# Kernel tuning notes

Hardware: AMD Instinct MI355X
Metric: run time of the kernel (lower is better)

Reference implementation:

```python
import jax, jax.numpy as jnp
import numpy as np

B, S, H = 4, 256, 768
NUM_BASIC = 4
NUM_REL = 32            # labels 1..31 are real edges, 0 = no edge
NUM_ALL = 2 * NUM_REL   # bidir: forward slots 0..31, reverse slots 33..63


def setup_inputs() -> dict:
    key = jax.random.key(0)
    k1, k2, k3, k4, k5 = jax.random.split(key, 5)
    hidden_states = jax.random.normal(k1, (B, S, H), dtype=jnp.float32)
    rels = jax.random.randint(k2, (B, S, S), 0, NUM_REL, dtype=jnp.int32)
    # xavier-ish init scale for params
    basic_matrix = jax.random.normal(k3, (NUM_BASIC, H, H), dtype=jnp.float32) * 0.02
    rel_weight = jax.random.normal(k4, (NUM_ALL, NUM_BASIC), dtype=jnp.float32) * 0.1
    self_weight = jax.random.normal(k5, (H, H), dtype=jnp.float32) * 0.02  # Linear weight (out,in)
    return {"hidden_states": hidden_states, "rels": rels,
            "basic_matrix": basic_matrix, "rel_weight": rel_weight,
            "self_weight": self_weight}


def reference(hidden_states, rels, basic_matrix, rel_weight, self_weight):
    dt = hidden_states.dtype
    # forward-direction one-hot relation tensor [B, NUM_ALL, S, S], masked where rels == 0
    fwd_mask = (rels > 0).astype(dt)                                   # [B,S,S]
    fwd_oh = jax.nn.one_hot(rels, NUM_ALL, axis=1, dtype=dt) * fwd_mask[:, None]
    # reverse direction (bidir): labels shifted by NUM_REL, zeroed where no edge
    rev_rels_raw = jnp.transpose(rels, (0, 2, 1))
    rev_rels = jnp.where(rev_rels_raw > 0, rev_rels_raw + NUM_REL, 0)  # {0} U {33..63}
    rev_mask = (rev_rels > 0).astype(dt)
    rev_oh = jax.nn.one_hot(rev_rels, NUM_ALL, axis=1, dtype=dt) * rev_mask[:, None]
    rel_tensor = fwd_oh + rev_oh                                       # [B,R,S,S]

    # basis decomposition: per-relation transform [R, H, H]
    rel_matrix = jnp.einsum('rb,bio->rio', rel_weight, basic_matrix)
    # per-relation transformed hidden states [B,R,S,H]
    r_hidden = jnp.einsum('bsi,rio->brso', hidden_states, rel_matrix)
    # adjacency aggregation [B,R,S,H]
    r_ctx = jnp.einsum('brij,brjo->brio', rel_tensor, r_hidden)
    # mean over neighbors (clamp count at 1)
    num_neighbors = jnp.maximum(rel_tensor.sum(-1), 1.0)               # [B,R,S]
    r_ctx = r_ctx / num_neighbors[..., None]
    context = r_ctx.sum(axis=1)                                        # [B,S,H]
    self_layer = hidden_states @ self_weight.T
    return self_layer + context
```

## Files before the change

kernel.cpp:

```cpp
#include <hip/hip_runtime.h>
#include <stdint.h>

typedef unsigned short u16;
typedef unsigned int u32;
typedef __attribute__((ext_vector_type(8))) short short8;
typedef __attribute__((ext_vector_type(4))) float float4v;

#define Bb 4
#define Ss 256
#define Hh 768
#define NBASIC 4
#define NALL 64

__device__ __forceinline__ float b2f(u16 h) {
    u32 u = ((u32)h) << 16;
    float f;
    __builtin_memcpy(&f, &u, 4);
    return f;
}
__device__ __forceinline__ u16 f2b(float f) {
    u32 u;
    __builtin_memcpy(&u, &f, 4);
    u = (u + 0x7fffu + ((u >> 16) & 1u)) >> 16;
    return (u16)u;
}

__device__ __forceinline__ int detect_bf16(const u32* __restrict__ hw) {
    int cnt = 0;
#pragma unroll
    for (int k = 0; k < 64; ++k) {
        const int e = (int)((hw[k] >> 7) & 0xFFu);
        cnt += (e >= 100 && e <= 140) ? 1 : 0;
    }
    return cnt >= 40;
}

__global__ __launch_bounds__(256) void k_prep(const void* __restrict__ h_raw,
                                              const void* __restrict__ basic_raw,
                                              const void* __restrict__ selfw_raw,
                                              const void* __restrict__ relw_raw,
                                              const int* __restrict__ rels,
                                              u16* __restrict__ hbf,
                                              u16* __restrict__ swbf,
                                              u16* __restrict__ basicT,
                                              u16* __restrict__ hT,
                                              u16* __restrict__ coefC) {
    __shared__ u16 tile[32][33];
    __shared__ float srelw[256];
    __shared__ u32 hist[NALL];

    const int blk = blockIdx.x;
    const int t = threadIdx.x;
    const int bf = detect_bf16((const u32*)h_raw);

    if (blk < 3072) {
        const int i = blk * 256 + t;
        hbf[i] = bf ? ((const u16*)h_raw)[i] : f2b(((const float*)h_raw)[i]);
    } else if (blk < 5376) {
        const int i = (blk - 3072) * 256 + t;
        swbf[i] = bf ? ((const u16*)selfw_raw)[i] : f2b(((const float*)selfw_raw)[i]);
    } else if (blk < 7680) {
        const int r = blk - 5376;
        const int o0 = (r % 24) * 32, i0 = ((r / 24) % 24) * 32, q = r / 576;
        const int tx = t & 31, ty = t >> 5;
        const size_t base = (size_t)q * Hh * Hh;
#pragma unroll
        for (int rr = 0; rr < 4; ++rr) {
            const size_t idx = base + (size_t)(i0 + ty + 8 * rr) * Hh + o0 + tx;
            tile[ty + 8 * rr][tx] = bf ? ((const u16*)basic_raw)[idx]
                                       : f2b(((const float*)basic_raw)[idx]);
        }
        __syncthreads();
#pragma unroll
        for (int rr = 0; rr < 4; ++rr)
            basicT[base + (size_t)(o0 + ty + 8 * rr) * Hh + i0 + tx] = tile[tx][ty + 8 * rr];
    } else if (blk < 8448) {
        const int r = blk - 7680;
        const int o0 = (r % 24) * 32, i0 = ((r / 24) % 8) * 32, b = r / 192;
        const int tx = t & 31, ty = t >> 5;
#pragma unroll
        for (int rr = 0; rr < 4; ++rr) {
            const size_t idx = ((size_t)b * Ss + i0 + ty + 8 * rr) * Hh + o0 + tx;
            tile[ty + 8 * rr][tx] = bf ? ((const u16*)h_raw)[idx]
                                       : f2b(((const float*)h_raw)[idx]);
        }
        __syncthreads();
#pragma unroll
        for (int rr = 0; rr < 4; ++rr)
            hT[((size_t)b * Hh + o0 + ty + 8 * rr) * Ss + i0 + tx] = tile[tx][ty + 8 * rr];
    } else {
        const int r = blk - 8448;
        const int i = r & 255, b = r >> 8;
        srelw[t] = bf ? b2f(((const u16*)relw_raw)[t]) : ((const float*)relw_raw)[t];
        if (t < NALL) hist[t] = 0u;
        __syncthreads();
        const int rf = rels[(b * Ss + i) * Ss + t];
        const int rc = rels[(b * Ss + t) * Ss + i];
        if (rf > 0) atomicAdd(&hist[rf], 1u);
        if (rc > 0) atomicAdd(&hist[rc + 32], 1u);
        __syncthreads();
        float c0 = 0.f, c1 = 0.f, c2 = 0.f, c3 = 0.f;
        if (rf > 0) {
            const float inv = 1.0f / (float)hist[rf];
            c0 += srelw[rf * 4 + 0] * inv; c1 += srelw[rf * 4 + 1] * inv;
            c2 += srelw[rf * 4 + 2] * inv; c3 += srelw[rf * 4 + 3] * inv;
        }
        if (rc > 0) {
            const int rr = rc + 32;
            const float inv = 1.0f / (float)hist[rr];
            c0 += srelw[rr * 4 + 0] * inv; c1 += srelw[rr * 4 + 1] * inv;
            c2 += srelw[rr * 4 + 2] * inv; c3 += srelw[rr * 4 + 3] * inv;
        }
        const size_t base = ((size_t)(b * 4) * Ss + i) * Ss + t;
        coefC[base]                    = f2b(c0);
        coefC[base + (size_t)Ss * Ss]     = f2b(c1);
        coefC[base + (size_t)2 * Ss * Ss] = f2b(c2);
        coefC[base + (size_t)3 * Ss * Ss] = f2b(c3);
    }
}

__global__ __launch_bounds__(256) void k_gemmP(const u16* __restrict__ coefC,
                                               const u16* __restrict__ hT,
                                               u16* __restrict__ pooled) {
    constexpr int LDT = 72;
    __shared__ u16 As[64 * LDT];
    __shared__ u16 Bs[64 * LDT];

    const int bk = blockIdx.z;
    const int b = bk >> 2;
    const int i0 = blockIdx.y * 64;
    const int o0 = blockIdx.x * 64;
    const int t = threadIdx.x;
    const int row = t >> 2, kk = (t & 3) * 16;
    const int w = t >> 6, l = t & 63, quad = l >> 4, l16 = l & 15;

    float4v acc[4];
#pragma unroll
    for (int c = 0; c < 4; ++c) acc[c] = (float4v){0.f, 0.f, 0.f, 0.f};

    const u16* aB = coefC + ((size_t)bk * Ss + i0 + row) * Ss + kk;
    const u16* bB = hT + ((size_t)b * Hh + o0 + row) * Ss + kk;

    uint4 a0 = *(const uint4*)aB;
    uint4 a1 = *(const uint4*)(aB + 8);
    uint4 b0 = *(const uint4*)bB;
    uint4 b1 = *(const uint4*)(bB + 8);

    for (int s = 0; s < 4; ++s) {
        __syncthreads();
        *(uint4*)(&As[row * LDT + kk]) = a0;
        *(uint4*)(&As[row * LDT + kk + 8]) = a1;
        *(uint4*)(&Bs[row * LDT + kk]) = b0;
        *(uint4*)(&Bs[row * LDT + kk + 8]) = b1;
        __syncthreads();
        if (s + 1 < 4) {
            a0 = *(const uint4*)(aB + (s + 1) * 64);
            a1 = *(const uint4*)(aB + (s + 1) * 64 + 8);
            b0 = *(const uint4*)(bB + (s + 1) * 64);
            b1 = *(const uint4*)(bB + (s + 1) * 64 + 8);
        }
#pragma unroll
        for (int k2 = 0; k2 < 64; k2 += 32) {
            const short8 af = *(const short8*)(&As[(16 * w + l16) * LDT + k2 + quad * 8]);
#pragma unroll
            for (int c = 0; c < 4; ++c) {
                const short8 bfr = *(const short8*)(&Bs[(16 * c + l16) * LDT + k2 + quad * 8]);
                acc[c] = __builtin_amdgcn_mfma_f32_16x16x32_bf16(af, bfr, acc[c], 0, 0, 0);
            }
        }
    }

#pragma unroll
    for (int c = 0; c < 4; ++c)
#pragma unroll
        for (int r = 0; r < 4; ++r) {
            const int il = 16 * w + quad * 4 + r;
            const int ol = 16 * c + l16;
            pooled[((size_t)bk * Ss + i0 + il) * Hh + o0 + ol] = f2b(acc[c][r]);
        }
}

__global__ __launch_bounds__(256) void k_gemmO(const u16* __restrict__ hbf,
                                               const u16* __restrict__ pooled,
                                               const u16* __restrict__ basicT,
                                               const u16* __restrict__ swbf,
                                               float* __restrict__ partial) {
    constexpr int LDT = 72;
    __shared__ u16 As[64 * LDT];
    __shared__ u16 Bs[64 * LDT];

    const int z = blockIdx.z;
    const int b = z & 3, q = z >> 2;
    const int i0 = blockIdx.y * 64;
    const int o0 = blockIdx.x * 64;
    const int t = threadIdx.x;
    const int row = t >> 2, kk = (t & 3) * 16;
    const int w = t >> 6, l = t & 63, quad = l >> 4, l16 = l & 15;

    float4v acc[4];
#pragma unroll
    for (int c = 0; c < 4; ++c) acc[c] = (float4v){0.f, 0.f, 0.f, 0.f};

    const u16* aB = (q < 4) ? pooled + (((size_t)(b * 4 + q)) * Ss + i0 + row) * Hh + kk
                            : hbf + ((size_t)b * Ss + i0 + row) * Hh + kk;
    const u16* bB = (q < 4) ? basicT + ((size_t)q * Hh + o0 + row) * Hh + kk
                            : swbf + (size_t)(o0 + row) * Hh + kk;

    uint4 a0 = *(const uint4*)aB;
    uint4 a1 = *(const uint4*)(aB + 8);
    uint4 b0 = *(const uint4*)bB;
    uint4 b1 = *(const uint4*)(bB + 8);

    for (int s = 0; s < 12; ++s) {
        __syncthreads();
        *(uint4*)(&As[row * LDT + kk]) = a0;
        *(uint4*)(&As[row * LDT + kk + 8]) = a1;
        *(uint4*)(&Bs[row * LDT + kk]) = b0;
        *(uint4*)(&Bs[row * LDT + kk + 8]) = b1;
        __syncthreads();
        if (s + 1 < 12) {
            a0 = *(const uint4*)(aB + (s + 1) * 64);
            a1 = *(const uint4*)(aB + (s + 1) * 64 + 8);
            b0 = *(const uint4*)(bB + (s + 1) * 64);
            b1 = *(const uint4*)(bB + (s + 1) * 64 + 8);
        }
#pragma unroll
        for (int k2 = 0; k2 < 64; k2 += 32) {
            const short8 af = *(const short8*)(&As[(16 * w + l16) * LDT + k2 + quad * 8]);
#pragma unroll
            for (int c = 0; c < 4; ++c) {
                const short8 bfr = *(const short8*)(&Bs[(16 * c + l16) * LDT + k2 + quad * 8]);
                acc[c] = __builtin_amdgcn_mfma_f32_16x16x32_bf16(af, bfr, acc[c], 0, 0, 0);
            }
        }
    }

#pragma unroll
    for (int c = 0; c < 4; ++c)
#pragma unroll
        for (int r = 0; r < 4; ++r) {
            const int il = 16 * w + quad * 4 + r;
            const int ol = 16 * c + l16;
            partial[((size_t)z * Ss + i0 + il) * Hh + o0 + ol] = acc[c][r];
        }
}

__global__ __launch_bounds__(256) void k_reduce(const float* __restrict__ partial,
                                                const void* __restrict__ h_raw,
                                                void* __restrict__ outv) {
    const int bf = detect_bf16((const u32*)h_raw);
    const size_t idx = ((size_t)blockIdx.x * 256 + threadIdx.x) * 4;
    const size_t slice = (size_t)Bb * Ss * Hh;
    float4 s = *(const float4*)(partial + idx);
#pragma unroll
    for (int q = 1; q < 5; ++q) {
        const float4 p = *(const float4*)(partial + q * slice + idx);
        s.x += p.x; s.y += p.y; s.z += p.z; s.w += p.w;
    }
    if (bf) {
        const u32 lo = (u32)f2b(s.x) | ((u32)f2b(s.y) << 16);
        const u32 hi = (u32)f2b(s.z) | ((u32)f2b(s.w) << 16);
        *(uint2*)((u16*)outv + idx) = make_uint2(lo, hi);
    } else {
        *(float4*)((float*)outv + idx) = s;
    }
}

extern "C" void kernel_launch(void* const* d_in, const int* in_sizes, int n_in,
                              void* d_out, int out_size, void* d_ws, size_t ws_size,
                              hipStream_t stream) {
    const void* h_raw = d_in[0];
    const int* rels = (const int*)d_in[1];
    const void* basic_raw = d_in[2];
    const void* relw_raw = d_in[3];
    const void* selfw_raw = d_in[4];

    u16* pooled = (u16*)d_ws;
    u16* basicT = pooled + (size_t)Bb * 4 * Ss * Hh;
    u16* hbf    = basicT + (size_t)NBASIC * Hh * Hh;
    u16* hT     = hbf + (size_t)Bb * Ss * Hh;
    u16* swbf   = hT + (size_t)Bb * Hh * Ss;
    u16* coefC  = swbf + (size_t)Hh * Hh;
    float* partial = (float*)(coefC + (size_t)Bb * 4 * Ss * Ss);

    k_prep<<<9472, 256, 0, stream>>>(h_raw, basic_raw, selfw_raw, relw_raw, rels,
                                     hbf, swbf, basicT, hT, coefC);
    k_gemmP<<<dim3(12, 4, 16), 256, 0, stream>>>(coefC, hT, pooled);
    k_gemmO<<<dim3(12, 4, 20), 256, 0, stream>>>(hbf, pooled, basicT, swbf, partial);
    k_reduce<<<768, 256, 0, stream>>>(partial, h_raw, d_out);
}
```

Measured before the change: 116.0 us.

## Fuse prep, both GEMMs and reduction into one persistent kernel with grid barriers

Replaces the four separate launches with a single persistent kernel of 512 blocks. Each block walks the work items of every stage in a grid-stride loop, and the stages are separated by software grid barriers built from atomic counters in the workspace. It also reuses the raw bf16 inputs directly when the input is bf16, which skips the conversion copies. The aim is to remove launch gaps and tail effects between stages, at the cost of relying on all blocks being co-resident. The barrier counters are reset inside the kernel while a magic flag persists across calls, so repeated invocations risk a race.

After: 352.4 us. +203.8%, slower.

```diff
diff --git a/kernel.cpp b/kernel.cpp
--- a/kernel.cpp
+++ b/kernel.cpp
@@ -11,6 +11,8 @@
 #define Hh 768
 #define NBASIC 4
 #define NALL 64
+#define GRID 512
+#define MAGIC 0x1234ABCD
 
 __device__ __forceinline__ float b2f(u16 h) {
     u32 u = ((u32)h) << 16;
@@ -35,125 +37,40 @@
     return cnt >= 40;
 }
 
-__global__ __launch_bounds__(256) void k_prep(const void* __restrict__ h_raw,
-                                              const void* __restrict__ basic_raw,
-                                              const void* __restrict__ selfw_raw,
-                                              const void* __restrict__ relw_raw,
-                                              const int* __restrict__ rels,
-                                              u16* __restrict__ hbf,
-                                              u16* __restrict__ swbf,
-                                              u16* __restrict__ basicT,
-                                              u16* __restrict__ hT,
-                                              u16* __restrict__ coefC) {
-    __shared__ u16 tile[32][33];
-    __shared__ float srelw[256];
-    __shared__ u32 hist[NALL];
-
-    const int blk = blockIdx.x;
-    const int t = threadIdx.x;
-    const int bf = detect_bf16((const u32*)h_raw);
-
-    if (blk < 3072) {
-        const int i = blk * 256 + t;
-        hbf[i] = bf ? ((const u16*)h_raw)[i] : f2b(((const float*)h_raw)[i]);
-    } else if (blk < 5376) {
-        const int i = (blk - 3072) * 256 + t;
-        swbf[i] = bf ? ((const u16*)selfw_raw)[i] : f2b(((const float*)selfw_raw)[i]);
-    } else if (blk < 7680) {
-        const int r = blk - 5376;
-        const int o0 = (r % 24) * 32, i0 = ((r / 24) % 24) * 32, q = r / 576;
-        const int tx = t & 31, ty = t >> 5;
-        const size_t base = (size_t)q * Hh * Hh;
-#pragma unroll
-        for (int rr = 0; rr < 4; ++rr) {
-            const size_t idx = base + (size_t)(i0 + ty + 8 * rr) * Hh + o0 + tx;
-            tile[ty + 8 * rr][tx] = bf ? ((const u16*)basic_raw)[idx]
-                                       : f2b(((const float*)basic_raw)[idx]);
-        }
-        __syncthreads();
-#pragma unroll
-        for (int rr = 0; rr < 4; ++rr)
-            basicT[base + (size_t)(o0 + ty + 8 * rr) * Hh + i0 + tx] = tile[tx][ty + 8 * rr];
-    } else if (blk < 8448) {
-        const int r = blk - 7680;
-        const int o0 = (r % 24) * 32, i0 = ((r / 24) % 8) * 32, b = r / 192;
-        const int tx = t & 31, ty = t >> 5;
-#pragma unroll
-        for (int rr = 0; rr < 4; ++rr) {
-            const size_t idx = ((size_t)b * Ss + i0 + ty + 8 * rr) * Hh + o0 + tx;
-            tile[ty + 8 * rr][tx] = bf ? ((const u16*)h_raw)[idx]
-                                       : f2b(((const float*)h_raw)[idx]);
-        }
-        __syncthreads();
-#pragma unroll
-        for (int rr = 0; rr < 4; ++rr)
-            hT[((size_t)b * Hh + o0 + ty + 8 * rr) * Ss + i0 + tx] = tile[tx][ty + 8 * rr];
-    } else {
-        const int r = blk - 8448;
-        const int i = r & 255, b = r >> 8;
-        srelw[t] = bf ? b2f(((const u16*)relw_raw)[t]) : ((const float*)relw_raw)[t];
-        if (t < NALL) hist[t] = 0u;
-        __syncthreads();
-        const int rf = rels[(b * Ss + i) * Ss + t];
-        const int rc = rels[(b * Ss + t) * Ss + i];
-        if (rf > 0) atomicAdd(&hist[rf], 1u);
-        if (rc > 0) atomicAdd(&hist[rc + 32], 1u);
-        __syncthreads();
-        float c0 = 0.f, c1 = 0.f, c2 = 0.f, c3 = 0.f;
-        if (rf > 0) {
-            const float inv = 1.0f / (float)hist[rf];
-            c0 += srelw[rf * 4 + 0] * inv; c1 += srelw[rf * 4 + 1] * inv;
-            c2 += srelw[rf * 4 + 2] * inv; c3 += srelw[rf * 4 + 3] * inv;
-        }
-        if (rc > 0) {
-            const int rr = rc + 32;
-            const float inv = 1.0f / (float)hist[rr];
-            c0 += srelw[rr * 4 + 0] * inv; c1 += srelw[rr * 4 + 1] * inv;
-            c2 += srelw[rr * 4 + 2] * inv; c3 += srelw[rr * 4 + 3] * inv;
-        }
-        const size_t base = ((size_t)(b * 4) * Ss + i) * Ss + t;
-        coefC[base]                    = f2b(c0);
-        coefC[base + (size_t)Ss * Ss]     = f2b(c1);
-        coefC[base + (size_t)2 * Ss * Ss] = f2b(c2);
-        coefC[base + (size_t)3 * Ss * Ss] = f2b(c3);
-    }
-}
-
-__global__ __launch_bounds__(256) void k_gemmP(const u16* __restrict__ coefC,
-                                               const u16* __restrict__ hT,
-                                               u16* __restrict__ pooled) {
-    constexpr int LDT = 72;
-    __shared__ u16 As[64 * LDT];
-    __shared__ u16 Bs[64 * LDT];
-
-    const int bk = blockIdx.z;
-    const int b = bk >> 2;
-    const int i0 = blockIdx.y * 64;
-    const int o0 = blockIdx.x * 64;
-    const int t = threadIdx.x;
+__device__ __forceinline__ void gbar(int* bar, int idx) {
+    __syncthreads();
+    if (threadIdx.x == 0) {
+        __threadfence();
+        while (__hip_atomic_load(&bar[0], __ATOMIC_ACQUIRE, __HIP_MEMORY_SCOPE_AGENT) != MAGIC)
+            __builtin_amdgcn_s_sleep(2);
+        __hip_atomic_fetch_add(&bar[1 + idx], 1, __ATOMIC_ACQ_REL, __HIP_MEMORY_SCOPE_AGENT);
+        while (__hip_atomic_load(&bar[1 + idx], __ATOMIC_ACQUIRE, __HIP_MEMORY_SCOPE_AGENT) < GRID)
+            __builtin_amdgcn_s_sleep(2);
+        __threadfence();
+    }
+    __syncthreads();
+}
+
+__device__ __forceinline__ void gemm_tile(const u16* __restrict__ aB,
+                                          const u16* __restrict__ bB,
+                                          int niter, u16* As, u16* Bs,
+                                          float4v* acc, int t) {
     const int row = t >> 2, kk = (t & 3) * 16;
     const int w = t >> 6, l = t & 63, quad = l >> 4, l16 = l & 15;
-
-    float4v acc[4];
 #pragma unroll
     for (int c = 0; c < 4; ++c) acc[c] = (float4v){0.f, 0.f, 0.f, 0.f};
-
-    const u16* aB = coefC + ((size_t)bk * Ss + i0 + row) * Ss + kk;
-    const u16* bB = hT + ((size_t)b * Hh + o0 + row) * Ss + kk;
-
     uint4 a0 = *(const uint4*)aB;
     uint4 a1 = *(const uint4*)(aB + 8);
     uint4 b0 = *(const uint4*)bB;
     uint4 b1 = *(const uint4*)(bB + 8);
-
-    for (int s = 0; s < 4; ++s) {
+    for (int s = 0; s < niter; ++s) {
         __syncthreads();
-        *(uint4*)(&As[row * LDT + kk]) = a0;
-        *(uint4*)(&As[row * LDT + kk + 8]) = a1;
-        *(uint4*)(&Bs[row * LDT + kk]) = b0;
-        *(uint4*)(&Bs[row * LDT + kk + 8]) = b1;
+        *(uint4*)(&As[row * 72 + kk]) = a0;
+        *(uint4*)(&As[row * 72 + kk + 8]) = a1;
+        *(uint4*)(&Bs[row * 72 + kk]) = b0;
+        *(uint4*)(&Bs[row * 72 + kk + 8]) = b1;
         __syncthreads();
-        if (s + 1 < 4) {
+        if (s + 1 < niter) {
             a0 = *(const uint4*)(aB + (s + 1) * 64);
             a1 = *(const uint4*)(aB + (s + 1) * 64 + 8);
             b0 = *(const uint4*)(bB + (s + 1) * 64);
@@ -161,108 +78,188 @@
         }
 #pragma unroll
         for (int k2 = 0; k2 < 64; k2 += 32) {
-            const short8 af = *(const short8*)(&As[(16 * w + l16) * LDT + k2 + quad * 8]);
+            const short8 af = *(const short8*)(&As[(16 * w + l16) * 72 + k2 + quad * 8]);
 #pragma unroll
             for (int c = 0; c < 4; ++c) {
-                const short8 bfr = *(const short8*)(&Bs[(16 * c + l16) * LDT + k2 + quad * 8]);
+                const short8 bfr = *(const short8*)(&Bs[(16 * c + l16) * 72 + k2 + quad * 8]);
                 acc[c] = __builtin_amdgcn_mfma_f32_16x16x32_bf16(af, bfr, acc[c], 0, 0, 0);
             }
         }
     }
-
-#pragma unroll
-    for (int c = 0; c < 4; ++c)
-#pragma unroll
-        for (int r = 0; r < 4; ++r) {
-            const int il = 16 * w + quad * 4 + r;
-            const int ol = 16 * c + l16;
-            pooled[((size_t)bk * Ss + i0 + il) * Hh + o0 + ol] = f2b(acc[c][r]);
-        }
-}
-
-__global__ __launch_bounds__(256) void k_gemmO(const u16* __restrict__ hbf,
-                                               const u16* __restrict__ pooled,
-                                               const u16* __restrict__ basicT,
-                                               const u16* __restrict__ swbf,
-                                               float* __restrict__ partial) {
-    constexpr int LDT = 72;
-    __shared__ u16 As[64 * LDT];
-    __shared__ u16 Bs[64 * LDT];
-
-    const int z = blockIdx.z;
-    const int b = z & 3, q = z >> 2;
-    const int i0 = blockIdx.y * 64;
-    const int o0 = blockIdx.x * 64;
+}
+
+__global__ __launch_bounds__(256, 2) void k_all(const void* __restrict__ h_raw,
+                                                const int* __restrict__ rels,
+                                                const void* __restrict__ basic_raw,
+                                                const void* __restrict__ relw_raw,
+                                                const void* __restrict__ selfw_raw,
+                                                u16* __restrict__ pooled,
+                                                u16* __restrict__ basicT,
+                                                u16* __restrict__ hbf,
+                                                u16* __restrict__ hT,
+                                                u16* __restrict__ swbf,
+                                                u16* __restrict__ coefC,
+                                                float* __restrict__ partial,
+                                                int* __restrict__ bar,
+                                                void* __restrict__ outv) {
+    __shared__ __align__(16) u16 As[64 * 72];
+    __shared__ __align__(16) u16 Bs[64 * 72];
+
     const int t = threadIdx.x;
-    const int row = t >> 2, kk = (t & 3) * 16;
-    const int w = t >> 6, l = t & 63, quad = l >> 4, l16 = l & 15;
-
-    float4v acc[4];
-#pragma unroll
-    for (int c = 0; c < 4; ++c) acc[c] = (float4v){0.f, 0.f, 0.f, 0.f};
-
-    const u16* aB = (q < 4) ? pooled + (((size_t)(b * 4 + q)) * Ss + i0 + row) * Hh + kk
-                            : hbf + ((size_t)b * Ss + i0 + row) * Hh + kk;
-    const u16* bB = (q < 4) ? basicT + ((size_t)q * Hh + o0 + row) * Hh + kk
-                            : swbf + (size_t)(o0 + row) * Hh + kk;
-
-    uint4 a0 = *(const uint4*)aB;
-    uint4 a1 = *(const uint4*)(aB + 8);
-    uint4 b0 = *(const uint4*)bB;
-    uint4 b1 = *(const uint4*)(bB + 8);
-
-    for (int s = 0; s < 12; ++s) {
-        __syncthreads();
-        *(uint4*)(&As[row * LDT + kk]) = a0;
-        *(uint4*)(&As[row * LDT + kk + 8]) = a1;
-        *(uint4*)(&Bs[row * LDT + kk]) = b0;
-        *(uint4*)(&Bs[row * LDT + kk + 8]) = b1;
-        __syncthreads();
-        if (s + 1 < 12) {
-            a0 = *(const uint4*)(aB + (s + 1) * 64);
-            a1 = *(const uint4*)(aB + (s + 1) * 64 + 8);
-            b0 = *(const uint4*)(bB + (s + 1) * 64);
-            b1 = *(const uint4*)(bB + (s + 1) * 64 + 8);
-        }
-#pragma unroll
-        for (int k2 = 0; k2 < 64; k2 += 32) {
-            const short8 af = *(const short8*)(&As[(16 * w + l16) * LDT + k2 + quad * 8]);
-#pragma unroll
-            for (int c = 0; c < 4; ++c) {
-                const short8 bfr = *(const short8*)(&Bs[(16 * c + l16) * LDT + k2 + quad * 8]);
-                acc[c] = __builtin_amdgcn_mfma_f32_16x16x32_bf16(af, bfr, acc[c], 0, 0, 0);
-            }
-        }
-    }
-
-#pragma unroll
-    for (int c = 0; c < 4; ++c)
-#pragma unroll
-        for (int r = 0; r < 4; ++r) {
-            const int il = 16 * w + quad * 4 + r;
-            const int ol = 16 * c + l16;
-            partial[((size_t)z * Ss + i0 + il) * Hh + o0 + ol] = acc[c][r];
-        }
-}
-
-__global__ __launch_bounds__(256) void k_reduce(const float* __restrict__ partial,
-                                                const void* __restrict__ h_raw,
-                                                void* __restrict__ outv) {
     const int bf = detect_bf16((const u32*)h_raw);
-    const size_t idx = ((size_t)blockIdx.x * 256 + threadIdx.x) * 4;
-    const size_t slice = (size_t)Bb * Ss * Hh;
-    float4 s = *(const float4*)(partial + idx);
-#pragma unroll
-    for (int q = 1; q < 5; ++q) {
-        const float4 p = *(const float4*)(partial + q * slice + idx);
-        s.x += p.x; s.y += p.y; s.z += p.z; s.w += p.w;
-    }
-    if (bf) {
-        const u32 lo = (u32)f2b(s.x) | ((u32)f2b(s.y) << 16);
-        const u32 hi = (u32)f2b(s.z) | ((u32)f2b(s.w) << 16);
-        *(uint2*)((u16*)outv + idx) = make_uint2(lo, hi);
-    } else {
-        *(float4*)((float*)outv + idx) = s;
+
+    if (blockIdx.x == 0 && t == 0) {
+        __hip_atomic_store(&bar[1], 0, __ATOMIC_RELAXED, __HIP_MEMORY_SCOPE_AGENT);
+        __hip_atomic_store(&bar[2], 0, __ATOMIC_RELAXED, __HIP_MEMORY_SCOPE_AGENT);
+        __hip_atomic_store(&bar[3], 0, __ATOMIC_RELAXED, __HIP_MEMORY_SCOPE_AGENT);
+        __hip_atomic_store(&bar[0], MAGIC, __ATOMIC_RELEASE, __HIP_MEMORY_SCOPE_AGENT);
+    }
+
+    {
+        u16(*tile)[33] = (u16(*)[33])As;
+        float* srelw = (float*)Bs;
+        u32* hist = (u32*)(Bs + 1024);
+        const int nA = bf ? 4096 : 9472;
+        for (int u = blockIdx.x; u < nA; u += GRID) {
+            __syncthreads();
+            if (u < 2304) {
+                const int r = u;
+                const int o0 = (r % 24) * 32, i0 = ((r / 24) % 24) * 32, q = r / 576;
+                const int tx = t & 31, ty = t >> 5;
+                const size_t base = (size_t)q * Hh * Hh;
+#pragma unroll
+                for (int rr = 0; rr < 4; ++rr) {
+                    const size_t idx = base + (size_t)(i0 + ty + 8 * rr) * Hh + o0 + tx;
+                    tile[ty + 8 * rr][tx] = bf ? ((const u16*)basic_raw)[idx]
+                                               : f2b(((const float*)basic_raw)[idx]);
+                }
+                __syncthreads();
+#pragma unroll
+                for (int rr = 0; rr < 4; ++rr)
+                    basicT[base + (size_t)(o0 + ty + 8 * rr) * Hh + i0 + tx] = tile[tx][ty + 8 * rr];
+            } else if (u < 3072) {
+                const int r = u - 2304;
+                const int o0 = (r % 24) * 32, i0 = ((r / 24) % 8) * 32, b = r / 192;
+                const int tx = t & 31, ty = t >> 5;
+#pragma unroll
+                for (int rr = 0; rr < 4; ++rr) {
+                    const size_t idx = ((size_t)b * Ss + i0 + ty + 8 * rr) * Hh + o0 + tx;
+                    tile[ty + 8 * rr][tx] = bf ? ((const u16*)h_raw)[idx]
+                                               : f2b(((const float*)h_raw)[idx]);
+                }
+                __syncthreads();
+#pragma unroll
+                for (int rr = 0; rr < 4; ++rr)
+                    hT[((size_t)b * Hh + o0 + ty + 8 * rr) * Ss + i0 + tx] = tile[tx][ty + 8 * rr];
+            } else if (u < 4096) {
+                const int r = u - 3072;
+                const int i = r & 255, b = r >> 8;
+                srelw[t] = bf ? b2f(((const u16*)relw_raw)[t]) : ((const float*)relw_raw)[t];
+                if (t < NALL) hist[t] = 0u;
+                __syncthreads();
+                const int rfw = rels[(b * Ss + i) * Ss + t];
+                const int rcl = rels[(b * Ss + t) * Ss + i];
+                if (rfw > 0) atomicAdd(&hist[rfw], 1u);
+                if (rcl > 0) atomicAdd(&hist[rcl + 32], 1u);
+                __syncthreads();
+                float c0 = 0.f, c1 = 0.f, c2 = 0.f, c3 = 0.f;
+                if (rfw > 0) {
+                    const float inv = 1.0f / (float)hist[rfw];
+                    c0 += srelw[rfw * 4 + 0] * inv; c1 += srelw[rfw * 4 + 1] * inv;
+                    c2 += srelw[rfw * 4 + 2] * inv; c3 += srelw[rfw * 4 + 3] * inv;
+                }
+                if (rcl > 0) {
+                    const int rr = rcl + 32;
+                    const float inv = 1.0f / (float)hist[rr];
+                    c0 += srelw[rr * 4 + 0] * inv; c1 += srelw[rr * 4 + 1] * inv;
+                    c2 += srelw[rr * 4 + 2] * inv; c3 += srelw[rr * 4 + 3] * inv;
+                }
+                const size_t base = ((size_t)(b * 4) * Ss + i) * Ss + t;
+                coefC[base] = f2b(c0);
+                coefC[base + (size_t)Ss * Ss] = f2b(c1);
+                coefC[base + (size_t)2 * Ss * Ss] = f2b(c2);
+                coefC[base + (size_t)3 * Ss * Ss] = f2b(c3);
+            } else if (u < 7168) {
+                const int i = (u - 4096) * 256 + t;
+                hbf[i] = f2b(((const float*)h_raw)[i]);
+            } else {
+                const int i = (u - 7168) * 256 + t;
+                swbf[i] = f2b(((const float*)selfw_raw)[i]);
+            }
+        }
+    }
+    gbar(bar, 0);
+
+    {
+        const int row = t >> 2, kk = (t & 3) * 16;
+        const int w = t >> 6, l = t & 63, quad = l >> 4, l16 = l & 15;
+        for (int u = blockIdx.x; u < 768; u += GRID) {
+            const int o0 = (u % 12) * 64;
+            const int i0 = ((u / 12) % 4) * 64;
+            const int bk = u / 48;
+            const int b = bk >> 2;
+            const u16* aB = coefC + ((size_t)bk * Ss + i0 + row) * Ss + kk;
+            const u16* bB = hT + ((size_t)b * Hh + o0 + row) * Ss + kk;
+            float4v acc[4];
+            gemm_tile(aB, bB, 4, As, Bs, acc, t);
+#pragma unroll
+            for (int c = 0; c < 4; ++c)
+#pragma unroll
+                for (int r = 0; r < 4; ++r) {
+                    const int il = 16 * w + quad * 4 + r;
+                    const int ol = 16 * c + l16;
+                    pooled[((size_t)bk * Ss + i0 + il) * Hh + o0 + ol] = f2b(acc[c][r]);
+                }
+        }
+    }
+    gbar(bar, 1);
+
+    {
+        const u16* heff = bf ? (const u16*)h_raw : hbf;
+        const u16* seff = bf ? (const u16*)selfw_raw : swbf;
+        const int row = t >> 2, kk = (t & 3) * 16;
+        const int w = t >> 6, l = t & 63, quad = l >> 4, l16 = l & 15;
+        for (int u = blockIdx.x; u < 960; u += GRID) {
+            const int o0 = (u % 12) * 64;
+            const int i0 = ((u / 12) % 4) * 64;
+            const int z = u / 48;
+            const int b = z & 3, q = z >> 2;
+            const u16* aB = (q < 4) ? pooled + (((size_t)(b * 4 + q)) * Ss + i0 + row) * Hh + kk
+                                    : heff + ((size_t)b * Ss + i0 + row) * Hh + kk;
+            const u16* bB = (q < 4) ? basicT + ((size_t)q * Hh + o0 + row) * Hh + kk
+                                    : seff + (size_t)(o0 + row) * Hh + kk;
+            float4v acc[4];
+            gemm_tile(aB, bB, 12, As, Bs, acc, t);
+#pragma unroll
+            for (int c = 0; c < 4; ++c)
+#pragma unroll
+                for (int r = 0; r < 4; ++r) {
+                    const int il = 16 * w + quad * 4 + r;
+                    const int ol = 16 * c + l16;
+                    partial[((size_t)z * Ss + i0 + il) * Hh + o0 + ol] = acc[c][r];
+                }
+        }
+    }
+    gbar(bar, 2);
+
+    {
+        const size_t slice = (size_t)Bb * Ss * Hh;
+        for (int u = blockIdx.x; u < 768; u += GRID) {
+            const size_t idx = ((size_t)u * 256 + t) * 4;
+            float4 s = *(const float4*)(partial + idx);
+#pragma unroll
+            for (int q = 1; q < 5; ++q) {
+                const float4 p = *(const float4*)(partial + q * slice + idx);
+                s.x += p.x; s.y += p.y; s.z += p.z; s.w += p.w;
+            }
+            if (bf) {
+                const u32 lo = (u32)f2b(s.x) | ((u32)f2b(s.y) << 16);
+                const u32 hi = (u32)f2b(s.z) | ((u32)f2b(s.w) << 16);
+                *(uint2*)((u16*)outv + idx) = make_uint2(lo, hi);
+            } else {
+                *(float4*)((float*)outv + idx) = s;
+            }
+        }
     }
 }
 
@@ -282,10 +279,9 @@
     u16* swbf   = hT + (size_t)Bb * Hh * Ss;
     u16* coefC  = swbf + (size_t)Hh * Hh;
     float* partial = (float*)(coefC + (size_t)Bb * 4 * Ss * Ss);
-
-    k_prep<<<9472, 256, 0, stream>>>(h_raw, basic_raw, selfw_raw, relw_raw, rels,
-                                     hbf, swbf, basicT, hT, coefC);
-    k_gemmP<<<dim3(12, 4, 16), 256, 0, stream>>>(coefC, hT, pooled);
-    k_gemmO<<<dim3(12, 4, 20), 256, 0, stream>>>(hbf, pooled, basicT, swbf, partial);
-    k_reduce<<<768, 256, 0, stream>>>(partial, h_raw, d_out);
-}
+    int* bar = (int*)(partial + (size_t)5 * Bb * Ss * Hh);
+
+    k_all<<<GRID, 256, 0, stream>>>(h_raw, rels, basic_raw, relw_raw, selfw_raw,
+                                    pooled, basicT, hbf, hT, swbf, coefC,
+                                    partial, bar, d_out);
+}
```
